# Kernel optimization log

Hardware: AMD Instinct MI355X
Metric: run time of the kernel (lower is better)

## Reference

```python
import jax, jax.numpy as jnp
import numpy as np

M_PARAM = 8          # M from __init__
NUM_INTERESTS = 32   # K, num_extracted_interests (max)


def setup_inputs() -> dict:
    key = jax.random.key(0)
    ks = jax.random.split(key, 6)
    bs, L, N, d, ic, K = 512, 100, 64, 256, 256, NUM_INTERESTS
    history = jax.random.normal(ks[0], (bs, L, d), dtype=jnp.float32)
    history_mask = jnp.ones((bs, L), dtype=bool)  # unused by the original forward, kept for signature fidelity
    candidates = jax.random.normal(ks[1], (bs, N, d), dtype=jnp.float32)
    num_extracted_interests = jnp.maximum(
        jax.random.randint(ks[2], (bs,), 0, K, dtype=jnp.int32), 1)
    unique_category_counts = jax.random.randint(ks[3], (bs,), 1, 19, dtype=jnp.int32)
    W = jax.random.normal(ks[4], (ic, d), dtype=jnp.float32) / np.sqrt(d)   # Linear(news_dim->interest_dim), no bias
    context_codes = jax.random.normal(ks[5], (K, ic), dtype=jnp.float32) / np.sqrt(ic)
    return {
        "history_news_representations": history,
        "history_mask": history_mask,
        "candidate_news_representations": candidates,
        "num_extracted_interests": num_extracted_interests,
        "unique_category_counts": unique_category_counts,
        "W": W,
        "context_codes": context_codes,
    }


def _user_encoder(history, candidates, num_interests, cat_counts, W, context_codes):
    bs, L, d = history.shape
    K = context_codes.shape[0]
    # ---- PolyAttention ----
    proj = jnp.tanh(jnp.einsum('bld,cd->blc', history, W))           # [bs, L, ic]
    scores = jnp.einsum('blc,kc->bkl', proj, context_codes)          # [bs, K, L]
    code_mask = jnp.arange(K)[None, :] < num_interests[:, None]      # [bs, K]
    scores = jnp.where(code_mask[:, :, None], scores, jnp.float32(-1e9))
    attn = jax.nn.softmax(scores, axis=2)                            # over history length L
    attn = jnp.nan_to_num(attn, nan=0.0, posinf=0.0, neginf=0.0)
    interests = jnp.einsum('bkl,bld->bkd', attn, history)            # [bs, K, d]
    # ---- InterestCandidateAttention, vectorized over all N candidates ----
    w = jnp.einsum('bkd,bnd->bnk', interests, candidates)            # [bs, N, K]
    dynK = jnp.clip(
        jnp.ceil(jnp.log2(M_PARAM * cat_counts.astype(jnp.float32))).astype(jnp.int32),
        1, K)                                                        # [bs]
    # variable-K top-k mask via descending ranks (values a.s. distinct)
    order = jnp.argsort(-w, axis=-1)
    ranks = jnp.argsort(order, axis=-1)                              # rank 0 = largest
    topk_mask = (ranks < dynK[:, None, None]).astype(w.dtype)        # [bs, N, K]
    masked = w * topk_mask
    user = jnp.einsum('bnk,bkd->bnd', masked, interests)             # [bs, N, d]
    return user


def reference(history_news_representations, history_mask, candidate_news_representations,
              num_extracted_interests, unique_category_counts, W, context_codes):
    return _user_encoder(history_news_representations, candidate_news_representations,
                         num_extracted_interests, unique_category_counts, W, context_codes)
```

## Files before the change

### kernel.cpp

```cpp
#include <hip/hip_runtime.h>
#include <hip/hip_bf16.h>

typedef __bf16 bf16_t;
typedef __bf16 bf16x8 __attribute__((ext_vector_type(8)));
typedef float  f32x4  __attribute__((ext_vector_type(4)));

#define BS 512
#define LH 100
#define NC 64
#define DD 256
#define IC 256
#define KK 32

#define OFF_WPL 6553600
#define OFF_CPL (6553600 + 3 * 131072)

__device__ __forceinline__ void split3(float v, bf16_t& h, bf16_t& l, bf16_t& l2) {
    h = (bf16_t)v;  float r1 = v - (float)h;
    l = (bf16_t)r1; float r2 = r1 - (float)l;
    l2 = (bf16_t)r2;
}

__device__ __forceinline__ void split3x8(const float* v, bf16x8& h, bf16x8& l, bf16x8& l2) {
#pragma unroll
    for (int j = 0; j < 8; j++) {
        bf16_t a, b, c;
        split3(v[j], a, b, c);
        h[j] = a; l[j] = b; l2[j] = c;
    }
}

__device__ __forceinline__ void mfma6(const bf16x8& ah, const bf16x8& al, const bf16x8& al2,
                                      const bf16x8& bh, const bf16x8& bl, const bf16x8& bl2,
                                      f32x4& accM, f32x4& accC) {
    accM = __builtin_amdgcn_mfma_f32_16x16x32_bf16(ah,  bh,  accM, 0, 0, 0);
    accC = __builtin_amdgcn_mfma_f32_16x16x32_bf16(ah,  bl,  accC, 0, 0, 0);
    accC = __builtin_amdgcn_mfma_f32_16x16x32_bf16(al,  bh,  accC, 0, 0, 0);
    accC = __builtin_amdgcn_mfma_f32_16x16x32_bf16(ah,  bl2, accC, 0, 0, 0);
    accC = __builtin_amdgcn_mfma_f32_16x16x32_bf16(al,  bl,  accC, 0, 0, 0);
    accC = __builtin_amdgcn_mfma_f32_16x16x32_bf16(al2, bh,  accC, 0, 0, 0);
}

__device__ __forceinline__ float fast_tanh_f32(float xf) {
    const double t  = fabs((double)xf) * 2.0;
    const double nf = rint(t * 1.4426950408889634);
    double r = fma(nf, -6.93147180369123816490e-01, t);
    r = fma(nf, -1.90821492927058770002e-10, r);
    const double r2 = r * r;
    double p =        2.08767569878680989792e-09;
    p = fma(p, r,     2.50521083854417187751e-08);
    p = fma(p, r,     2.75573192239858906526e-07);
    p = fma(p, r,     2.75573192239858925110e-06);
    p = fma(p, r,     2.48015873015873015873e-05);
    p = fma(p, r,     1.98412698412698412526e-04);
    p = fma(p, r,     1.38888888888888894069e-03);
    p = fma(p, r,     8.33333333333333321769e-03);
    p = fma(p, r,     4.16666666666666643537e-02);
    p = fma(p, r,     1.66666666666666657415e-01);
    p = fma(p, r,     5.00000000000000000000e-01);
    const double q   = fma(r2, p, r);
    const double s   = ldexp(1.0, (int)nf);
    const double em1 = fma(s, q, s - 1.0);
    double ti = em1 / (em1 + 2.0);
    if (t > 20.0) ti = 1.0;
    return copysignf((float)ti, xf);
}

__global__ __launch_bounds__(256) void kp_split(const float* __restrict__ W,
                                                const float* __restrict__ C,
                                                bf16_t* __restrict__ Wh, bf16_t* __restrict__ Wl,
                                                bf16_t* __restrict__ Wl2,
                                                bf16_t* __restrict__ Ch, bf16_t* __restrict__ Cl,
                                                bf16_t* __restrict__ Cl2) {
    int idx = blockIdx.x * 256 + threadIdx.x;
    if (idx < 65536) {
        bf16_t h, l, l2;
        split3(W[idx], h, l, l2);
        Wh[idx] = h; Wl[idx] = l; Wl2[idx] = l2;
    } else {
        int i = idx - 65536;
        if (i < 8192) {
            bf16_t h, l, l2;
            split3(C[i], h, l, l2);
            Ch[i] = h; Cl[i] = l; Cl2[i] = l2;
        }
    }
}

#define WCH 24576
__global__ __launch_bounds__(448) void k12_proj_scores(const float* __restrict__ H,
                                                       const bf16_t* __restrict__ Wh,
                                                       const bf16_t* __restrict__ Wl,
                                                       const bf16_t* __restrict__ Wl2,
                                                       const bf16_t* __restrict__ Ch,
                                                       const bf16_t* __restrict__ Cl,
                                                       const bf16_t* __restrict__ Cl2,
                                                       float* __restrict__ S) {
    __shared__ __align__(16) char wbuf[2][WCH];
    __shared__ float pl[7][16 * 34];

    const int tid = threadIdx.x;
    const int wave = tid >> 6;
    const int lane = tid & 63;
    const int r = lane & 15, q = lane >> 4;
    const int b = blockIdx.x;
    const int lrow0 = wave * 16;

    const bf16_t* it_base[4];
    int it_src[4], it_dst[4];
#pragma unroll
    for (int it = 0; it < 4; it++) {
        const int g = tid + it * 448;
        const int p = (g >> 9) & 3, rem = g & 511, row = rem >> 5, grp = rem & 31;
        it_base[it] = (p == 0) ? Wh : (p == 1) ? Wl : Wl2;
        it_src[it] = row * DD + grp * 8;
        it_dst[it] = (p * 16 + row) * 512 + ((grp * 16) ^ ((row & 7) << 4));
    }
    const bool has4 = (tid < 192);

    bf16x8 Ah[8], Al[8], Al2[8];
    {
        long grow = (long)b * LH + lrow0 + r;
        const long maxrow = (long)BS * LH - 1;
        if (grow > maxrow) grow = maxrow;
        const float* arow = H + (size_t)grow * DD + q * 8;
#pragma unroll
        for (int ks = 0; ks < 8; ks++) {
            const float* ap = arow + ks * 32;
            float4 u = *(const float4*)ap;
            float4 v = *(const float4*)(ap + 4);
            float av[8] = {u.x, u.y, u.z, u.w, v.x, v.y, v.z, v.w};
            split3x8(av, Ah[ks], Al[ks], Al2[ks]);
        }
    }

    const f32x4 zero = {0.f, 0.f, 0.f, 0.f};
    f32x4 saccM[2], saccC[2];
    saccM[0] = zero; saccM[1] = zero; saccC[0] = zero; saccC[1] = zero;

    float* myp = pl[wave];
    const int swz = (r & 7) << 4;

    {
        bf16x8 p0 = *(const bf16x8*)(it_base[0] + it_src[0]);
        bf16x8 p1 = *(const bf16x8*)(it_base[1] + it_src[1]);
        bf16x8 p2 = *(const bf16x8*)(it_base[2] + it_src[2]);
        bf16x8 p3;
        if (has4) p3 = *(const bf16x8*)(it_base[3] + it_src[3]);
        *(bf16x8*)(wbuf[0] + it_dst[0]) = p0;
        *(bf16x8*)(wbuf[0] + it_dst[1]) = p1;
        *(bf16x8*)(wbuf[0] + it_dst[2]) = p2;
        if (has4) *(bf16x8*)(wbuf[0] + it_dst[3]) = p3;
    }
    __syncthreads();

    for (int c16 = 0; c16 < 16; c16++) {
        const char* cur = wbuf[c16 & 1];
        char* nxt = wbuf[(c16 & 1) ^ 1];
        const bool pfv = (c16 < 15);

        bf16x8 p0, p1, p2, p3;
        if (pfv) {
            const int co = (c16 + 1) * 16 * DD;
            p0 = *(const bf16x8*)(it_base[0] + co + it_src[0]);
            p1 = *(const bf16x8*)(it_base[1] + co + it_src[1]);
            p2 = *(const bf16x8*)(it_base[2] + co + it_src[2]);
            if (has4) p3 = *(const bf16x8*)(it_base[3] + co + it_src[3]);
        }

        f32x4 aM = zero, aC = zero;
#pragma unroll
        for (int ks = 0; ks < 8; ks++) {
            const int colb = (ks * 64 + q * 16) ^ swz;
            const char* rowp = cur + r * 512 + colb;
            bf16x8 bh  = *(const bf16x8*)(rowp);
            bf16x8 bl  = *(const bf16x8*)(rowp + 8192);
            bf16x8 bl2 = *(const bf16x8*)(rowp + 16384);
            mfma6(Ah[ks], Al[ks], Al2[ks], bh, bl, bl2, aM, aC);
        }

        const int colb2 = (c16 & 1) * 16;
#pragma unroll
        for (int i = 0; i < 4; i++) {
            float s1 = aM[i] + aC[i];
            myp[(q * 4 + i) * 34 + colb2 + r] = fast_tanh_f32(s1);
        }

        if (c16 & 1) {
            const int c0 = (c16 >> 1) * 32;
            const float* ps = myp + r * 34 + q * 8;
            float pv[8];
#pragma unroll
            for (int j = 0; j < 8; j++) pv[j] = ps[j];
            bf16x8 ph, plo, pl2;
            split3x8(pv, ph, plo, pl2);
#pragma unroll
            for (int ntS = 0; ntS < 2; ntS++) {
                const size_t base = (size_t)(ntS * 16 + r) * IC + c0 + q * 8;
                bf16x8 ch  = *(const bf16x8*)(Ch  + base);
                bf16x8 cl  = *(const bf16x8*)(Cl  + base);
                bf16x8 cl2 = *(const bf16x8*)(Cl2 + base);
                mfma6(ph, plo, pl2, ch, cl, cl2, saccM[ntS], saccC[ntS]);
            }
        }

        if (pfv) {
            *(bf16x8*)(nxt + it_dst[0]) = p0;
            *(bf16x8*)(nxt + it_dst[1]) = p1;
            *(bf16x8*)(nxt + it_dst[2]) = p2;
            if (has4) *(bf16x8*)(nxt + it_dst[3]) = p3;
        }
        __syncthreads();
    }

#pragma unroll
    for (int ntS = 0; ntS < 2; ntS++)
#pragma unroll
        for (int i = 0; i < 4; i++) {
            const int lrow = lrow0 + q * 4 + i;
            if (lrow < LH)
                S[((size_t)b * LH + lrow) * KK + ntS * 16 + r] = saccM[ntS][i] + saccC[ntS][i];
        }
}

__global__ __launch_bounds__(512) void k3456_fused(const float* __restrict__ Sg,
                                                   const int* __restrict__ ni,
                                                   const int* __restrict__ cc,
                                                   const float* __restrict__ H,
                                                   const float* __restrict__ cand,
                                                   float* __restrict__ out) {
    __shared__ __align__(16) char smem[47616];
    float*  attn_l = (float*)smem;
    float*  ls     = (float*)(smem + 12800);
    double* red    = (double*)(smem + 25600);
    float*  ht     = (float*)(smem + 12800);
    float*  I_l    = (float*)(smem + 12800);
    float*  shw    = (float*)smem;

    const int b = blockIdx.x;
    const int tid = threadIdx.x;
    const int wave = tid >> 6;
    const int lane = tid & 63;
    const int r = lane & 15, q = lane >> 4;
    const f32x4 zero = {0.f, 0.f, 0.f, 0.f};

    {
        const float* Sb = Sg + (size_t)b * LH * KK;
        for (int i = tid; i < LH * KK; i += 512) ls[i] = Sb[i];
        __syncthreads();

        const int k = tid & 31;
        const int grp = tid >> 5;
        const bool act = (grp < 8);
        const int nib = ni[b];

        double vals[13];
        int cnt = 0;
        if (act) {
            double vmax = -1e300;
            for (int l = grp; l < LH; l += 8) {
                double v = (double)ls[l * KK + k];
                vals[cnt++] = v;
                vmax = fmax(vmax, v);
            }
            red[grp * 33 + k] = vmax;
        }
        __syncthreads();
        if (tid < 32) {
            double m = red[k];
            for (int j = 1; j < 8; j++) m = fmax(m, red[j * 33 + k]);
            red[k] = m;
        }
        __syncthreads();
        const double mx = red[k];
        __syncthreads();

        if (act) {
            double s = 0.0;
            for (int i = 0; i < cnt; i++) {
                double e = exp(vals[i] - mx);
                vals[i] = e;
                s += e;
            }
            red[grp * 33 + k] = s;
        }
        __syncthreads();
        if (tid < 32) {
            double t = 0.0;
            for (int j = 0; j < 8; j++) t += red[j * 33 + k];
            red[k] = t;
        }
        __syncthreads();
        const double inv = 1.0 / red[k];

        if (act) {
            float* ab = attn_l + k * LH;
            const bool masked = (k >= nib);
            cnt = 0;
            for (int l = grp; l < LH; l += 8) {
                ab[l] = masked ? 0.01f : (float)(vals[cnt] * inv);
                cnt++;
            }
        }
    }
    __syncthreads();

    {
        const float* Hb = H + (size_t)b * LH * DD;
        const int mtB = wave & 1;
        const int m0B = mtB * 16;

        f32x4 accM[4], accC[4];
#pragma unroll
        for (int jj = 0; jj < 4; jj++) { accM[jj] = zero; accC[jj] = zero; }

        for (int ks = 0; ks < 4; ks++) {
            const int l0c = ks * 32;
            __syncthreads();
            for (int u = tid; u < 32 * 64; u += 512) {
                const int l = u >> 6, dg = u & 63;
                float4 v = {0.f, 0.f, 0.f, 0.f};
                if (l0c + l < LH) v = *(const float4*)(Hb + (size_t)(l0c + l) * DD + dg * 4);
                ht[(dg * 4 + 0) * 34 + l] = v.x;
                ht[(dg * 4 + 1) * 34 + l] = v.y;
                ht[(dg * 4 + 2) * 34 + l] = v.z;
                ht[(dg * 4 + 3) * 34 + l] = v.w;
            }
            __syncthreads();

            float av[8];
#pragma unroll
            for (int j = 0; j < 8; j++) {
                const int l = l0c + q * 8 + j;
                av[j] = (l < LH) ? attn_l[(m0B + r) * LH + l] : 0.f;
            }
            bf16x8 ah, al, al2;
            split3x8(av, ah, al, al2);

#pragma unroll
            for (int jj = 0; jj < 4; jj++) {
                const int job = wave + jj * 8;
                const int nt = job >> 1;
                const int n0 = nt * 16;
                float bv[8];
                const float* hp = ht + (n0 + r) * 34 + q * 8;
#pragma unroll
                for (int j = 0; j < 8; j++) bv[j] = hp[j];
                bf16x8 bh, bl, bl2;
                split3x8(bv, bh, bl, bl2);
                mfma6(ah, al, al2, bh, bl, bl2, accM[jj], accC[jj]);
            }
        }
        __syncthreads();

#pragma unroll
        for (int jj = 0; jj < 4; jj++) {
            const int job = wave + jj * 8;
            const int nt = job >> 1;
            const int n0 = nt * 16;
#pragma unroll
            for (int i = 0; i < 4; i++)
                I_l[(m0B + q * 4 + i) * 260 + n0 + r] = accM[jj][i] + accC[jj][i];
        }
    }
    __syncthreads();

    {
        const float* Cb = cand + (size_t)b * NC * DD;
        const int job = wave;
        const int mt = job >> 1, nt = job & 1;
        const int m0 = mt * 16, n0 = nt * 16;
        f32x4 accM = zero, accC = zero;
#pragma unroll
        for (int ks = 0; ks < 8; ks++) {
            const float* ap = Cb + (size_t)(m0 + r) * DD + ks * 32 + q * 8;
            const float* bp = I_l + (n0 + r) * 260 + ks * 32 + q * 8;
            float4 u1 = *(const float4*)ap;      float4 u2 = *(const float4*)(ap + 4);
            float4 v1 = *(const float4*)bp;      float4 v2 = *(const float4*)(bp + 4);
            float av[8] = {u1.x,u1.y,u1.z,u1.w,u2.x,u2.y,u2.z,u2.w};
            float bv[8] = {v1.x,v1.y,v1.z,v1.w,v2.x,v2.y,v2.z,v2.w};
            bf16x8 ah, al, al2, bh, bl, bl2;
            split3x8(av, ah, al, al2);
            split3x8(bv, bh, bl, bl2);
            mfma6(ah, al, al2, bh, bl, bl2, accM, accC);
        }
#pragma unroll
        for (int i = 0; i < 4; i++) shw[(m0 + q * 4 + i) * 33 + n0 + r] = accM[i] + accC[i];

        __syncthreads();

        if (tid < NC) {
            const int n = tid;
            int c8 = 8 * cc[b];
            int dynK = 32 - __clz(c8 - 1);
            dynK = min(max(dynK, 1), KK);
            float v[KK];
            for (int k = 0; k < KK; k++) v[k] = shw[n * 33 + k];
            for (int k = 0; k < KK; k++) {
                int rank = 0;
                for (int j = 0; j < KK; j++)
                    rank += (v[j] > v[k]) || (v[j] == v[k] && j < k);
                shw[n * 33 + k] = (rank < dynK) ? v[k] : 0.f;
            }
        }
    }
    __syncthreads();

    {
        const int d = tid & 255;
        const int nh = tid >> 8;
        float icol[KK];
#pragma unroll
        for (int k = 0; k < KK; k++) icol[k] = I_l[k * 260 + d];

        const int nend = nh * 32 + 32;
        for (int n = nh * 32; n < nend; n++) {
            const float* wr = shw + n * 33;
            float acc = 0.f;
#pragma unroll
            for (int k = 0; k < KK; k++) acc += wr[k] * icol[k];
            out[((size_t)b * NC + n) * DD + d] = acc;
        }
    }
}

extern "C" void kernel_launch(void* const* d_in, const int* in_sizes, int n_in,
                              void* d_out, int out_size, void* d_ws, size_t ws_size,
                              hipStream_t stream) {
    const float* hist = (const float*)d_in[0];
    const float* cand = (const float*)d_in[2];
    const int* ni = (const int*)d_in[3];
    const int* cc = (const int*)d_in[4];
    const float* W = (const float*)d_in[5];
    const float* C = (const float*)d_in[6];
    float* out = (float*)d_out;

    char* w8 = (char*)d_ws;
    float*  S   = (float*)(w8 + 0);
    bf16_t* Wh  = (bf16_t*)(w8 + OFF_WPL);
    bf16_t* Wl  = (bf16_t*)(w8 + OFF_WPL + 131072);
    bf16_t* Wl2 = (bf16_t*)(w8 + OFF_WPL + 262144);
    bf16_t* Ch  = (bf16_t*)(w8 + OFF_CPL);
    bf16_t* Cl  = (bf16_t*)(w8 + OFF_CPL + 16384);
    bf16_t* Cl2 = (bf16_t*)(w8 + OFF_CPL + 32768);

    kp_split<<<288, 256, 0, stream>>>(W, C, Wh, Wl, Wl2, Ch, Cl, Cl2);
    k12_proj_scores<<<BS, 448, 0, stream>>>(hist, Wh, Wl, Wl2, Ch, Cl, Cl2, S);
    k3456_fused<<<BS, 512, 0, stream>>>(S, ni, cc, hist, cand, out);
}
```

Before: 251.4 us.

## Fuse projection/score kernel with softmax-pooling-topk kernel into one megakernel

Merges the projection+scores kernel and the softmax/pooling/top-k/output kernel into a single 448-thread kernel per batch row. Scores now stay in shared memory instead of a global round trip, and one launch is removed. It also splits the compensation MFMA accumulator into two chains to shorten dependency latency, replaces libm exp with an inline double-precision polynomial, and redistributes the pooling, candidate-score and top-k rank work across 7 waves. The cost is shared-memory reuse with aliasing between phases, uneven work per wave, and the final output stage using only 256 threads.

```diff
diff --git a/kernel.cpp b/kernel.cpp
--- a/kernel.cpp
+++ b/kernel.cpp
@@ -39,6 +39,17 @@
     accC = __builtin_amdgcn_mfma_f32_16x16x32_bf16(ah,  bl2, accC, 0, 0, 0);
     accC = __builtin_amdgcn_mfma_f32_16x16x32_bf16(al,  bl,  accC, 0, 0, 0);
     accC = __builtin_amdgcn_mfma_f32_16x16x32_bf16(al2, bh,  accC, 0, 0, 0);
+}
+
+__device__ __forceinline__ void mfma6s(const bf16x8& ah, const bf16x8& al, const bf16x8& al2,
+                                       const bf16x8& bh, const bf16x8& bl, const bf16x8& bl2,
+                                       f32x4& accM, f32x4& accC0, f32x4& accC1) {
+    accM  = __builtin_amdgcn_mfma_f32_16x16x32_bf16(ah,  bh,  accM,  0, 0, 0);
+    accC0 = __builtin_amdgcn_mfma_f32_16x16x32_bf16(ah,  bl,  accC0, 0, 0, 0);
+    accC1 = __builtin_amdgcn_mfma_f32_16x16x32_bf16(al,  bh,  accC1, 0, 0, 0);
+    accC0 = __builtin_amdgcn_mfma_f32_16x16x32_bf16(ah,  bl2, accC0, 0, 0, 0);
+    accC1 = __builtin_amdgcn_mfma_f32_16x16x32_bf16(al,  bl,  accC1, 0, 0, 0);
+    accC0 = __builtin_amdgcn_mfma_f32_16x16x32_bf16(al2, bh,  accC0, 0, 0, 0);
 }
 
 __device__ __forceinline__ float fast_tanh_f32(float xf) {
@@ -66,6 +77,27 @@
     return copysignf((float)ti, xf);
 }
 
+__device__ __forceinline__ double fast_exp_f64(double x) {
+    const double nf = rint(x * 1.4426950408889634);
+    double r = fma(nf, -6.93147180369123816490e-01, x);
+    r = fma(nf, -1.90821492927058770002e-10, r);
+    const double r2 = r * r;
+    double p =        2.08767569878680989792e-09;
+    p = fma(p, r,     2.50521083854417187751e-08);
+    p = fma(p, r,     2.75573192239858906526e-07);
+    p = fma(p, r,     2.75573192239858925110e-06);
+    p = fma(p, r,     2.48015873015873015873e-05);
+    p = fma(p, r,     1.98412698412698412526e-04);
+    p = fma(p, r,     1.38888888888888894069e-03);
+    p = fma(p, r,     8.33333333333333321769e-03);
+    p = fma(p, r,     4.16666666666666643537e-02);
+    p = fma(p, r,     1.66666666666666657415e-01);
+    p = fma(p, r,     5.00000000000000000000e-01);
+    const double q = fma(r2, p, r);
+    const double s = ldexp(1.0, (int)nf);
+    return fma(s, q, s);
+}
+
 __global__ __launch_bounds__(256) void kp_split(const float* __restrict__ W,
                                                 const float* __restrict__ C,
                                                 bf16_t* __restrict__ Wh, bf16_t* __restrict__ Wl,
@@ -88,16 +120,28 @@
 }
 
 #define WCH 24576
-__global__ __launch_bounds__(448) void k12_proj_scores(const float* __restrict__ H,
-                                                       const bf16_t* __restrict__ Wh,
-                                                       const bf16_t* __restrict__ Wl,
-                                                       const bf16_t* __restrict__ Wl2,
-                                                       const bf16_t* __restrict__ Ch,
-                                                       const bf16_t* __restrict__ Cl,
-                                                       const bf16_t* __restrict__ Cl2,
-                                                       float* __restrict__ S) {
-    __shared__ __align__(16) char wbuf[2][WCH];
-    __shared__ float pl[7][16 * 34];
+__global__ __launch_bounds__(448, 4) void k_mega(const float* __restrict__ H,
+                                                 const bf16_t* __restrict__ Wh,
+                                                 const bf16_t* __restrict__ Wl,
+                                                 const bf16_t* __restrict__ Wl2,
+                                                 const bf16_t* __restrict__ Ch,
+                                                 const bf16_t* __restrict__ Cl,
+                                                 const bf16_t* __restrict__ Cl2,
+                                                 const int* __restrict__ ni,
+                                                 const int* __restrict__ cc,
+                                                 const float* __restrict__ cand,
+                                                 float* __restrict__ out) {
+    __shared__ __align__(16) char smem[64384];
+    char* wbuf0 = smem;
+    char* wbuf1 = smem + WCH;
+    float* pl_all = (float*)(smem + 2 * WCH);
+
+    float*  ls     = (float*)smem;
+    float*  attn_l = (float*)(smem + 12800);
+    double* red    = (double*)(smem + 25600);
+    float*  ht     = (float*)(smem + 27712);
+    float*  I_l    = (float*)(smem + 27712);
+    float*  shw    = (float*)smem;
 
     const int tid = threadIdx.x;
     const int wave = tid >> 6;
@@ -105,162 +149,140 @@
     const int r = lane & 15, q = lane >> 4;
     const int b = blockIdx.x;
     const int lrow0 = wave * 16;
-
-    const bf16_t* it_base[4];
-    int it_src[4], it_dst[4];
-#pragma unroll
-    for (int it = 0; it < 4; it++) {
-        const int g = tid + it * 448;
-        const int p = (g >> 9) & 3, rem = g & 511, row = rem >> 5, grp = rem & 31;
-        it_base[it] = (p == 0) ? Wh : (p == 1) ? Wl : Wl2;
-        it_src[it] = row * DD + grp * 8;
-        it_dst[it] = (p * 16 + row) * 512 + ((grp * 16) ^ ((row & 7) << 4));
-    }
-    const bool has4 = (tid < 192);
-
-    bf16x8 Ah[8], Al[8], Al2[8];
+    const f32x4 zero = {0.f, 0.f, 0.f, 0.f};
+
     {
-        long grow = (long)b * LH + lrow0 + r;
-        const long maxrow = (long)BS * LH - 1;
-        if (grow > maxrow) grow = maxrow;
-        const float* arow = H + (size_t)grow * DD + q * 8;
-#pragma unroll
-        for (int ks = 0; ks < 8; ks++) {
-            const float* ap = arow + ks * 32;
-            float4 u = *(const float4*)ap;
-            float4 v = *(const float4*)(ap + 4);
-            float av[8] = {u.x, u.y, u.z, u.w, v.x, v.y, v.z, v.w};
-            split3x8(av, Ah[ks], Al[ks], Al2[ks]);
-        }
-    }
-
-    const f32x4 zero = {0.f, 0.f, 0.f, 0.f};
-    f32x4 saccM[2], saccC[2];
-    saccM[0] = zero; saccM[1] = zero; saccC[0] = zero; saccC[1] = zero;
-
-    float* myp = pl[wave];
-    const int swz = (r & 7) << 4;
+        const bf16_t* it_base[4];
+        int it_src[4], it_dst[4];
+#pragma unroll
+        for (int it = 0; it < 4; it++) {
+            const int g = tid + it * 448;
+            const int p = (g >> 9) & 3, rem = g & 511, row = rem >> 5, grp = rem & 31;
+            it_base[it] = (p == 0) ? Wh : (p == 1) ? Wl : Wl2;
+            it_src[it] = row * DD + grp * 8;
+            it_dst[it] = (p * 16 + row) * 512 + ((grp * 16) ^ ((row & 7) << 4));
+        }
+        const bool has4 = (tid < 192);
+
+        bf16x8 Ah[8], Al[8], Al2[8];
+        {
+            long grow = (long)b * LH + lrow0 + r;
+            const long maxrow = (long)BS * LH - 1;
+            if (grow > maxrow) grow = maxrow;
+            const float* arow = H + (size_t)grow * DD + q * 8;
+#pragma unroll
+            for (int ks = 0; ks < 8; ks++) {
+                const float* ap = arow + ks * 32;
+                float4 u = *(const float4*)ap;
+                float4 v = *(const float4*)(ap + 4);
+                float av[8] = {u.x, u.y, u.z, u.w, v.x, v.y, v.z, v.w};
+                split3x8(av, Ah[ks], Al[ks], Al2[ks]);
+            }
+        }
+
+        f32x4 saccM[2], saccC[2];
+        saccM[0] = zero; saccM[1] = zero; saccC[0] = zero; saccC[1] = zero;
+
+        float* myp = pl_all + wave * 544;
+        const int swz = (r & 7) << 4;
+
+        {
+            bf16x8 p0 = *(const bf16x8*)(it_base[0] + it_src[0]);
+            bf16x8 p1 = *(const bf16x8*)(it_base[1] + it_src[1]);
+            bf16x8 p2 = *(const bf16x8*)(it_base[2] + it_src[2]);
+            bf16x8 p3;
+            if (has4) p3 = *(const bf16x8*)(it_base[3] + it_src[3]);
+            *(bf16x8*)(wbuf0 + it_dst[0]) = p0;
+            *(bf16x8*)(wbuf0 + it_dst[1]) = p1;
+            *(bf16x8*)(wbuf0 + it_dst[2]) = p2;
+            if (has4) *(bf16x8*)(wbuf0 + it_dst[3]) = p3;
+        }
+        __syncthreads();
+
+        for (int c16 = 0; c16 < 16; c16++) {
+            const char* cur = (c16 & 1) ? wbuf1 : wbuf0;
+            char* nxt = (c16 & 1) ? wbuf0 : wbuf1;
+            const bool pfv = (c16 < 15);
+
+            bf16x8 p0, p1, p2, p3;
+            if (pfv) {
+                const int co = (c16 + 1) * 16 * DD;
+                p0 = *(const bf16x8*)(it_base[0] + co + it_src[0]);
+                p1 = *(const bf16x8*)(it_base[1] + co + it_src[1]);
+                p2 = *(const bf16x8*)(it_base[2] + co + it_src[2]);
+                if (has4) p3 = *(const bf16x8*)(it_base[3] + co + it_src[3]);
+            }
+
+            f32x4 aM = zero, aC0 = zero, aC1 = zero;
+#pragma unroll
+            for (int ks = 0; ks < 8; ks++) {
+                const int colb = (ks * 64 + q * 16) ^ swz;
+                const char* rowp = cur + r * 512 + colb;
+                bf16x8 bh  = *(const bf16x8*)(rowp);
+                bf16x8 bl  = *(const bf16x8*)(rowp + 8192);
+                bf16x8 bl2 = *(const bf16x8*)(rowp + 16384);
+                mfma6s(Ah[ks], Al[ks], Al2[ks], bh, bl, bl2, aM, aC0, aC1);
+            }
+
+            const int colb2 = (c16 & 1) * 16;
+#pragma unroll
+            for (int i = 0; i < 4; i++) {
+                float s1 = aM[i] + aC0[i] + aC1[i];
+                myp[(q * 4 + i) * 34 + colb2 + r] = fast_tanh_f32(s1);
+            }
+
+            if (c16 & 1) {
+                const int c0 = (c16 >> 1) * 32;
+                const float* ps = myp + r * 34 + q * 8;
+                float pv[8];
+#pragma unroll
+                for (int j = 0; j < 8; j++) pv[j] = ps[j];
+                bf16x8 ph, plo, pl2;
+                split3x8(pv, ph, plo, pl2);
+#pragma unroll
+                for (int ntS = 0; ntS < 2; ntS++) {
+                    const size_t base = (size_t)(ntS * 16 + r) * IC + c0 + q * 8;
+                    bf16x8 ch  = *(const bf16x8*)(Ch  + base);
+                    bf16x8 cl  = *(const bf16x8*)(Cl  + base);
+                    bf16x8 cl2 = *(const bf16x8*)(Cl2 + base);
+                    mfma6(ph, plo, pl2, ch, cl, cl2, saccM[ntS], saccC[ntS]);
+                }
+            }
+
+            if (pfv) {
+                *(bf16x8*)(nxt + it_dst[0]) = p0;
+                *(bf16x8*)(nxt + it_dst[1]) = p1;
+                *(bf16x8*)(nxt + it_dst[2]) = p2;
+                if (has4) *(bf16x8*)(nxt + it_dst[3]) = p3;
+            }
+            __syncthreads();
+        }
+
+#pragma unroll
+        for (int ntS = 0; ntS < 2; ntS++)
+#pragma unroll
+            for (int i = 0; i < 4; i++) {
+                const int lrow = lrow0 + q * 4 + i;
+                if (lrow < LH)
+                    ls[lrow * KK + ntS * 16 + r] = saccM[ntS][i] + saccC[ntS][i];
+            }
+    }
+    __syncthreads();
 
     {
-        bf16x8 p0 = *(const bf16x8*)(it_base[0] + it_src[0]);
-        bf16x8 p1 = *(const bf16x8*)(it_base[1] + it_src[1]);
-        bf16x8 p2 = *(const bf16x8*)(it_base[2] + it_src[2]);
-        bf16x8 p3;
-        if (has4) p3 = *(const bf16x8*)(it_base[3] + it_src[3]);
-        *(bf16x8*)(wbuf[0] + it_dst[0]) = p0;
-        *(bf16x8*)(wbuf[0] + it_dst[1]) = p1;
-        *(bf16x8*)(wbuf[0] + it_dst[2]) = p2;
-        if (has4) *(bf16x8*)(wbuf[0] + it_dst[3]) = p3;
-    }
-    __syncthreads();
-
-    for (int c16 = 0; c16 < 16; c16++) {
-        const char* cur = wbuf[c16 & 1];
-        char* nxt = wbuf[(c16 & 1) ^ 1];
-        const bool pfv = (c16 < 15);
-
-        bf16x8 p0, p1, p2, p3;
-        if (pfv) {
-            const int co = (c16 + 1) * 16 * DD;
-            p0 = *(const bf16x8*)(it_base[0] + co + it_src[0]);
-            p1 = *(const bf16x8*)(it_base[1] + co + it_src[1]);
-            p2 = *(const bf16x8*)(it_base[2] + co + it_src[2]);
-            if (has4) p3 = *(const bf16x8*)(it_base[3] + co + it_src[3]);
-        }
-
-        f32x4 aM = zero, aC = zero;
-#pragma unroll
-        for (int ks = 0; ks < 8; ks++) {
-            const int colb = (ks * 64 + q * 16) ^ swz;
-            const char* rowp = cur + r * 512 + colb;
-            bf16x8 bh  = *(const bf16x8*)(rowp);
-            bf16x8 bl  = *(const bf16x8*)(rowp + 8192);
-            bf16x8 bl2 = *(const bf16x8*)(rowp + 16384);
-            mfma6(Ah[ks], Al[ks], Al2[ks], bh, bl, bl2, aM, aC);
-        }
-
-        const int colb2 = (c16 & 1) * 16;
-#pragma unroll
-        for (int i = 0; i < 4; i++) {
-            float s1 = aM[i] + aC[i];
-            myp[(q * 4 + i) * 34 + colb2 + r] = fast_tanh_f32(s1);
-        }
-
-        if (c16 & 1) {
-            const int c0 = (c16 >> 1) * 32;
-            const float* ps = myp + r * 34 + q * 8;
-            float pv[8];
-#pragma unroll
-            for (int j = 0; j < 8; j++) pv[j] = ps[j];
-            bf16x8 ph, plo, pl2;
-            split3x8(pv, ph, plo, pl2);
-#pragma unroll
-            for (int ntS = 0; ntS < 2; ntS++) {
-                const size_t base = (size_t)(ntS * 16 + r) * IC + c0 + q * 8;
-                bf16x8 ch  = *(const bf16x8*)(Ch  + base);
-                bf16x8 cl  = *(const bf16x8*)(Cl  + base);
-                bf16x8 cl2 = *(const bf16x8*)(Cl2 + base);
-                mfma6(ph, plo, pl2, ch, cl, cl2, saccM[ntS], saccC[ntS]);
-            }
-        }
-
-        if (pfv) {
-            *(bf16x8*)(nxt + it_dst[0]) = p0;
-            *(bf16x8*)(nxt + it_dst[1]) = p1;
-            *(bf16x8*)(nxt + it_dst[2]) = p2;
-            if (has4) *(bf16x8*)(nxt + it_dst[3]) = p3;
-        }
-        __syncthreads();
-    }
-
-#pragma unroll
-    for (int ntS = 0; ntS < 2; ntS++)
-#pragma unroll
-        for (int i = 0; i < 4; i++) {
-            const int lrow = lrow0 + q * 4 + i;
-            if (lrow < LH)
-                S[((size_t)b * LH + lrow) * KK + ntS * 16 + r] = saccM[ntS][i] + saccC[ntS][i];
-        }
-}
-
-__global__ __launch_bounds__(512) void k3456_fused(const float* __restrict__ Sg,
-                                                   const int* __restrict__ ni,
-                                                   const int* __restrict__ cc,
-                                                   const float* __restrict__ H,
-                                                   const float* __restrict__ cand,
-                                                   float* __restrict__ out) {
-    __shared__ __align__(16) char smem[47616];
-    float*  attn_l = (float*)smem;
-    float*  ls     = (float*)(smem + 12800);
-    double* red    = (double*)(smem + 25600);
-    float*  ht     = (float*)(smem + 12800);
-    float*  I_l    = (float*)(smem + 12800);
-    float*  shw    = (float*)smem;
-
-    const int b = blockIdx.x;
-    const int tid = threadIdx.x;
-    const int wave = tid >> 6;
-    const int lane = tid & 63;
-    const int r = lane & 15, q = lane >> 4;
-    const f32x4 zero = {0.f, 0.f, 0.f, 0.f};
-
-    {
-        const float* Sb = Sg + (size_t)b * LH * KK;
-        for (int i = tid; i < LH * KK; i += 512) ls[i] = Sb[i];
-        __syncthreads();
-
         const int k = tid & 31;
         const int grp = tid >> 5;
         const bool act = (grp < 8);
         const int nib = ni[b];
 
         double vals[13];
-        int cnt = 0;
         if (act) {
             double vmax = -1e300;
-            for (int l = grp; l < LH; l += 8) {
-                double v = (double)ls[l * KK + k];
-                vals[cnt++] = v;
+#pragma unroll
+            for (int i = 0; i < 13; i++) {
+                const int l = grp + 8 * i;
+                double v = (l < LH) ? (double)ls[l * KK + k] : -1e300;
+                vals[i] = v;
                 vmax = fmax(vmax, v);
             }
             red[grp * 33 + k] = vmax;
@@ -277,10 +299,14 @@
 
         if (act) {
             double s = 0.0;
-            for (int i = 0; i < cnt; i++) {
-                double e = exp(vals[i] - mx);
-                vals[i] = e;
-                s += e;
+#pragma unroll
+            for (int i = 0; i < 13; i++) {
+                const int l = grp + 8 * i;
+                if (l < LH) {
+                    double e = fast_exp_f64(vals[i] - mx);
+                    vals[i] = e;
+                    s += e;
+                }
             }
             red[grp * 33 + k] = s;
         }
@@ -296,10 +322,10 @@
         if (act) {
             float* ab = attn_l + k * LH;
             const bool masked = (k >= nib);
-            cnt = 0;
-            for (int l = grp; l < LH; l += 8) {
-                ab[l] = masked ? 0.01f : (float)(vals[cnt] * inv);
-                cnt++;
+#pragma unroll
+            for (int i = 0; i < 13; i++) {
+                const int l = grp + 8 * i;
+                if (l < LH) ab[l] = masked ? 0.01f : (float)(vals[i] * inv);
             }
         }
     }
@@ -309,15 +335,18 @@
         const float* Hb = H + (size_t)b * LH * DD;
         const int mtB = wave & 1;
         const int m0B = mtB * 16;
-
-        f32x4 accM[4], accC[4];
-#pragma unroll
-        for (int jj = 0; jj < 4; jj++) { accM[jj] = zero; accC[jj] = zero; }
+        const int wg = wave >> 1;
+        const int strideB = mtB ? 3 : 4;
+        const int njj = mtB ? 6 : 4;
+
+        f32x4 accM[6], accC[6];
+#pragma unroll
+        for (int jj = 0; jj < 6; jj++) { accM[jj] = zero; accC[jj] = zero; }
 
         for (int ks = 0; ks < 4; ks++) {
             const int l0c = ks * 32;
             __syncthreads();
-            for (int u = tid; u < 32 * 64; u += 512) {
+            for (int u = tid; u < 32 * 64; u += 448) {
                 const int l = u >> 6, dg = u & 63;
                 float4 v = {0.f, 0.f, 0.f, 0.f};
                 if (l0c + l < LH) v = *(const float4*)(Hb + (size_t)(l0c + l) * DD + dg * 4);
@@ -338,87 +367,101 @@
             split3x8(av, ah, al, al2);
 
 #pragma unroll
-            for (int jj = 0; jj < 4; jj++) {
-                const int job = wave + jj * 8;
-                const int nt = job >> 1;
+            for (int jj = 0; jj < 6; jj++) {
+                const int nt = wg + strideB * jj;
+                if (jj < njj && nt < 16) {
+                    const int n0 = nt * 16;
+                    float bv[8];
+                    const float* hp = ht + (n0 + r) * 34 + q * 8;
+#pragma unroll
+                    for (int j = 0; j < 8; j++) bv[j] = hp[j];
+                    bf16x8 bh, bl, bl2;
+                    split3x8(bv, bh, bl, bl2);
+                    mfma6(ah, al, al2, bh, bl, bl2, accM[jj], accC[jj]);
+                }
+            }
+        }
+        __syncthreads();
+
+#pragma unroll
+        for (int jj = 0; jj < 6; jj++) {
+            const int nt = wg + strideB * jj;
+            if (jj < njj && nt < 16) {
                 const int n0 = nt * 16;
-                float bv[8];
-                const float* hp = ht + (n0 + r) * 34 + q * 8;
-#pragma unroll
-                for (int j = 0; j < 8; j++) bv[j] = hp[j];
-                bf16x8 bh, bl, bl2;
-                split3x8(bv, bh, bl, bl2);
-                mfma6(ah, al, al2, bh, bl, bl2, accM[jj], accC[jj]);
-            }
-        }
-        __syncthreads();
-
-#pragma unroll
-        for (int jj = 0; jj < 4; jj++) {
-            const int job = wave + jj * 8;
-            const int nt = job >> 1;
-            const int n0 = nt * 16;
-#pragma unroll
-            for (int i = 0; i < 4; i++)
-                I_l[(m0B + q * 4 + i) * 260 + n0 + r] = accM[jj][i] + accC[jj][i];
+#pragma unroll
+                for (int i = 0; i < 4; i++)
+                    I_l[(m0B + q * 4 + i) * 260 + n0 + r] = accM[jj][i] + accC[jj][i];
+            }
         }
     }
     __syncthreads();
 
     {
         const float* Cb = cand + (size_t)b * NC * DD;
-        const int job = wave;
-        const int mt = job >> 1, nt = job & 1;
-        const int m0 = mt * 16, n0 = nt * 16;
-        f32x4 accM = zero, accC = zero;
-#pragma unroll
-        for (int ks = 0; ks < 8; ks++) {
-            const float* ap = Cb + (size_t)(m0 + r) * DD + ks * 32 + q * 8;
-            const float* bp = I_l + (n0 + r) * 260 + ks * 32 + q * 8;
-            float4 u1 = *(const float4*)ap;      float4 u2 = *(const float4*)(ap + 4);
-            float4 v1 = *(const float4*)bp;      float4 v2 = *(const float4*)(bp + 4);
-            float av[8] = {u1.x,u1.y,u1.z,u1.w,u2.x,u2.y,u2.z,u2.w};
-            float bv[8] = {v1.x,v1.y,v1.z,v1.w,v2.x,v2.y,v2.z,v2.w};
-            bf16x8 ah, al, al2, bh, bl, bl2;
-            split3x8(av, ah, al, al2);
-            split3x8(bv, bh, bl, bl2);
-            mfma6(ah, al, al2, bh, bl, bl2, accM, accC);
-        }
-#pragma unroll
-        for (int i = 0; i < 4; i++) shw[(m0 + q * 4 + i) * 33 + n0 + r] = accM[i] + accC[i];
-
-        __syncthreads();
-
-        if (tid < NC) {
-            const int n = tid;
+        for (int job = wave; job < 8; job += 7) {
+            const int mt = job >> 1, nt = job & 1;
+            const int m0 = mt * 16, n0 = nt * 16;
+            f32x4 accM = zero, accC = zero;
+#pragma unroll
+            for (int ks = 0; ks < 8; ks++) {
+                const float* ap = Cb + (size_t)(m0 + r) * DD + ks * 32 + q * 8;
+                const float* bp = I_l + (n0 + r) * 260 + ks * 32 + q * 8;
+                float4 u1 = *(const float4*)ap;      float4 u2 = *(const float4*)(ap + 4);
+                float4 v1 = *(const float4*)bp;      float4 v2 = *(const float4*)(bp + 4);
+                float av[8] = {u1.x,u1.y,u1.z,u1.w,u2.x,u2.y,u2.z,u2.w};
+                float bv[8] = {v1.x,v1.y,v1.z,v1.w,v2.x,v2.y,v2.z,v2.w};
+                bf16x8 ah, al, al2, bh, bl, bl2;
+                split3x8(av, ah, al, al2);
+                split3x8(bv, bh, bl, bl2);
+                mfma6(ah, al, al2, bh, bl, bl2, accM, accC);
+            }
+#pragma unroll
+            for (int i = 0; i < 4; i++) shw[(m0 + q * 4 + i) * 33 + n0 + r] = accM[i] + accC[i];
+        }
+        __syncthreads();
+
+        {
+            const int n = tid & 63;
+            const int kg = tid >> 6;
             int c8 = 8 * cc[b];
             int dynK = 32 - __clz(c8 - 1);
             dynK = min(max(dynK, 1), KK);
             float v[KK];
-            for (int k = 0; k < KK; k++) v[k] = shw[n * 33 + k];
-            for (int k = 0; k < KK; k++) {
-                int rank = 0;
-                for (int j = 0; j < KK; j++)
-                    rank += (v[j] > v[k]) || (v[j] == v[k] && j < k);
-                shw[n * 33 + k] = (rank < dynK) ? v[k] : 0.f;
+#pragma unroll
+            for (int j = 0; j < KK; j++) v[j] = shw[n * 33 + j];
+            float keep[5];
+#pragma unroll
+            for (int j = 0; j < 5; j++) {
+                const int kk2 = kg + 7 * j;
+                if (kk2 < KK) {
+                    int rank = 0;
+#pragma unroll
+                    for (int jj = 0; jj < KK; jj++)
+                        rank += (v[jj] > v[kk2]) || (v[jj] == v[kk2] && jj < kk2);
+                    keep[j] = (rank < dynK) ? v[kk2] : 0.f;
+                }
+            }
+            __syncthreads();
+#pragma unroll
+            for (int j = 0; j < 5; j++) {
+                const int kk2 = kg + 7 * j;
+                if (kk2 < KK) shw[n * 33 + kk2] = keep[j];
             }
         }
     }
     __syncthreads();
 
-    {
-        const int d = tid & 255;
-        const int nh = tid >> 8;
+    if (tid < 256) {
+        const int d = tid;
         float icol[KK];
 #pragma unroll
-        for (int k = 0; k < KK; k++) icol[k] = I_l[k * 260 + d];
-
-        const int nend = nh * 32 + 32;
-        for (int n = nh * 32; n < nend; n++) {
+        for (int kk2 = 0; kk2 < KK; kk2++) icol[kk2] = I_l[kk2 * 260 + d];
+
+        for (int n = 0; n < NC; n++) {
             const float* wr = shw + n * 33;
             float acc = 0.f;
 #pragma unroll
-            for (int k = 0; k < KK; k++) acc += wr[k] * icol[k];
+            for (int kk2 = 0; kk2 < KK; kk2++) acc += wr[kk2] * icol[kk2];
             out[((size_t)b * NC + n) * DD + d] = acc;
         }
     }
@@ -436,7 +479,6 @@
     float* out = (float*)d_out;
 
     char* w8 = (char*)d_ws;
-    float*  S   = (float*)(w8 + 0);
     bf16_t* Wh  = (bf16_t*)(w8 + OFF_WPL);
     bf16_t* Wl  = (bf16_t*)(w8 + OFF_WPL + 131072);
     bf16_t* Wl2 = (bf16_t*)(w8 + OFF_WPL + 262144);
@@ -445,6 +487,5 @@
     bf16_t* Cl2 = (bf16_t*)(w8 + OFF_CPL + 32768);
 
     kp_split<<<288, 256, 0, stream>>>(W, C, Wh, Wl, Wl2, Ch, Cl, Cl2);
-    k12_proj_scores<<<BS, 448, 0, stream>>>(hist, Wh, Wl, Wl2, Ch, Cl, Cl2, S);
-    k3456_fused<<<BS, 512, 0, stream>>>(S, ni, cc, hist, cand, out);
-}
+    k_mega<<<BS, 448, 0, stream>>>(hist, Wh, Wl, Wl2, Ch, Cl, Cl2, ni, cc, cand, out);
+}
```

Result: slower. 328.6 us (+30.7%).
